# Performance work log

Measured on AMD Instinct MI355X. Metric: run time of the kernel, lower is better.

## Reference

```python
import jax, jax.numpy as jnp
import numpy as np

B, R, N = 1, 1024, 128
C_FEAT, C_MSA, C_PAIR = 22, 256, 128
NBINS = 65  # relpos bins, vbins = arange(65) - 32


def setup_inputs() -> dict:
    key = jax.random.key(0)
    ks = jax.random.split(key, 9)
    w = lambda k, shape: (jax.random.normal(k, shape, jnp.float32) * 0.05)
    return {
        "target_feat": jax.random.normal(ks[0], (B, R, C_FEAT), jnp.float32),
        "residue_index": jnp.broadcast_to(jnp.arange(R, dtype=jnp.int32), (B, R)),
        "msa_feat": jax.random.normal(ks[1], (B, N, R, C_FEAT), jnp.float32),
        "Wa": w(ks[2], (C_PAIR, C_FEAT)), "ba": jnp.zeros((C_PAIR,), jnp.float32),
        "Wb": w(ks[3], (C_PAIR, C_FEAT)), "bb": jnp.zeros((C_PAIR,), jnp.float32),
        "Wm1": w(ks[4], (C_MSA, C_FEAT)), "bm1": jnp.zeros((C_MSA,), jnp.float32),
        "Wm2": w(ks[5], (C_MSA, C_FEAT)), "bm2": jnp.zeros((C_MSA,), jnp.float32),
        "Wpos": w(ks[6], (C_PAIR, NBINS)), "bpos": jnp.zeros((C_PAIR,), jnp.float32),
    }


def reference(target_feat, residue_index, msa_feat,
              Wa, ba, Wb, bb, Wm1, bm1, Wm2, bm2, Wpos, bpos):
    # pair init: z[b,i,j] = to_a(tf)[b,j] + to_b(tf)[b,i]
    a = target_feat @ Wa.T + ba                      # (b, r, c_pair)
    bv = target_feat @ Wb.T + bb                     # (b, r, c_pair)
    z = a[:, None, :, :] + bv[:, :, None, :]         # (b, r, r, c_pair)

    # relpos: nearest-bin one-hot of d = ri[j] - ri[i] against arange(65)-32,
    # then Linear(65 -> c_pair).  One-hot @ W.T is exactly an embedding gather
    # of row clip(d+32, 0, 64) from Wpos.T, so skip materializing the one-hot.
    d = residue_index[:, None, :] - residue_index[:, :, None]  # (b, r, r)
    bins = jnp.clip(d + (NBINS // 2), 0, NBINS - 1)            # (b, r, r) int
    z = z + Wpos.T[bins] + bpos                                # gather + bias

    # MSA init: m = to_m1(msa_feat) + to_m2(target_feat) broadcast over n rows
    m = (msa_feat @ Wm1.T + bm1) + (target_feat @ Wm2.T + bm2)[:, None, :, :]
    return m, z
```

## Files before the change

kernel.cpp:

```cpp
#include <hip/hip_runtime.h>

#define RR     1024
#define NSEQ   128
#define CFEAT  22
#define CMSA   256
#define CPAIR  128
#define NBINS  65

typedef float f4 __attribute__((ext_vector_type(4)));
typedef float f2 __attribute__((ext_vector_type(2)));

__global__ __launch_bounds__(256) void k_pre(
    const float* __restrict__ tf,
    const float* __restrict__ Wa, const float* __restrict__ ba,
    const float* __restrict__ Wb, const float* __restrict__ bb,
    const float* __restrict__ Wm2, const float* __restrict__ bm2,
    const float* __restrict__ Wpos, const float* __restrict__ bpos,
    float* __restrict__ a, float* __restrict__ bvp,
    float* __restrict__ tm2, float* __restrict__ pose)
{
    __shared__ float wlds[CFEAT][512];
    __shared__ float rows[8][CFEAT];
    const int t = threadIdx.x;
    const int r0 = blockIdx.x * 8;

    for (int idx = t; idx < 128 * CFEAT; idx += 256) {
        int c = idx / CFEAT, k = idx - c * CFEAT;
        wlds[k][c] = Wa[idx];
    }
    for (int idx = t; idx < 128 * CFEAT; idx += 256) {
        int c = idx / CFEAT, k = idx - c * CFEAT;
        wlds[k][128 + c] = Wb[idx];
    }
    for (int idx = t; idx < 256 * CFEAT; idx += 256) {
        int c = idx / CFEAT, k = idx - c * CFEAT;
        wlds[k][256 + c] = Wm2[idx];
    }
    for (int idx = t; idx < 8 * CFEAT; idx += 256) {
        int rr = idx / CFEAT, k = idx - rr * CFEAT;
        rows[rr][k] = tf[(r0 + rr) * CFEAT + k];
    }
    __syncthreads();

    #pragma unroll
    for (int rr = 0; rr < 8; ++rr) {
        const int r = r0 + rr;
        float s1 = 0.f, s2 = 0.f;
        #pragma unroll
        for (int k = 0; k < CFEAT; ++k) {
            float rv = rows[rr][k];
            s1 += rv * wlds[k][t];
            s2 += rv * wlds[k][256 + t];
        }
        tm2[r * CMSA + t] = s2 + bm2[t];
        if (t < CPAIR) a[r * CPAIR + t] = s1 + ba[t];
        else           bvp[r * CPAIR + (t - CPAIR)] = s1 + bb[t - CPAIR];
    }

    if (blockIdx.x < NBINS && t < CPAIR)
        pose[blockIdx.x * CPAIR + t] = Wpos[t * NBINS + blockIdx.x] + bpos[t];
}

#define PPB 64

__global__ __launch_bounds__(256, 8) void k_fused(
    const int* __restrict__ resi,
    const float* __restrict__ a, const float* __restrict__ bvp,
    const float* __restrict__ pose, float* __restrict__ out_z,
    const float* __restrict__ msa,
    const float* __restrict__ Wm1, const float* __restrict__ bm1,
    const float* __restrict__ tm2, float* __restrict__ out_m)
{
    __shared__ union U {
        struct { float rows[PPB][24]; } m;
        struct { int rj[512]; } p;
    } sm;
    const int bx = blockIdx.x;
    const int grp = bx >> 3, sub = bx & 7;
    const int id = (grp >> 1) * 8 + sub;
    const int t = threadIdx.x;

    if ((grp & 1) == 0) {
        const int i = id >> 1;
        const int jbase = (id & 1) * 512;
        for (int idx = t; idx < 512; idx += 256)
            sm.p.rj[idx] = resi[jbase + idx];
        __syncthreads();

        const int c4 = (t & 31) * 4;
        const int jo = t >> 5;
        const int ri = resi[i];
        const f4 bvv = *(const f4*)(bvp + (long)i * CPAIR + c4);
        float* dst = out_z + ((long)i * RR + jbase) * CPAIR;

        #pragma unroll 4
        for (int jj = 0; jj < 512; jj += 8) {
            const int jl = jj + jo;
            int d = sm.p.rj[jl] - ri + (NBINS / 2);
            d = min(max(d, 0), NBINS - 1);
            const f4 av = *(const f4*)(a + (long)(jbase + jl) * CPAIR + c4);
            const f4 pv = *(const f4*)(pose + (long)d * CPAIR + c4);
            f4 o = av + bvv + pv;
            __builtin_nontemporal_store(o, (f4*)(dst + (long)jl * CPAIR + c4));
        }
    } else {
        const long pbase = (long)id * PPB;
        const float* src = msa + pbase * CFEAT;
        for (int idx = t; idx < PPB * CFEAT; idx += 256) {
            int p = idx / CFEAT, k = idx - p * CFEAT;
            sm.m.rows[p][k] = src[idx];
        }
        if (t < PPB) { sm.m.rows[t][22] = 0.f; sm.m.rows[t][23] = 0.f; }

        const int c2 = (t & 127) * 2;
        const int ps = t >> 7;
        float wA[24], wB[24];
        const float* wp = Wm1 + (long)c2 * CFEAT;
        #pragma unroll
        for (int k = 0; k < CFEAT; ++k) { wA[k] = wp[k]; wB[k] = wp[CFEAT + k]; }
        wA[22] = wA[23] = wB[22] = wB[23] = 0.f;
        const float b0 = bm1[c2], b1 = bm1[c2 + 1];
        __syncthreads();

        for (int it = 0; it < PPB / 2; ++it) {
            const int p = it * 2 + ps;
            const long pair = pbase + p;
            const int r = (int)(pair & (RR - 1));
            float a0 = 0.f, a1 = 0.f;
            #pragma unroll
            for (int k4 = 0; k4 < 6; ++k4) {
                f4 mv = *(const f4*)&sm.m.rows[p][k4 * 4];
                a0 += mv.x * wA[k4 * 4 + 0]; a1 += mv.x * wB[k4 * 4 + 0];
                a0 += mv.y * wA[k4 * 4 + 1]; a1 += mv.y * wB[k4 * 4 + 1];
                a0 += mv.z * wA[k4 * 4 + 2]; a1 += mv.z * wB[k4 * 4 + 2];
                a0 += mv.w * wA[k4 * 4 + 3]; a1 += mv.w * wB[k4 * 4 + 3];
            }
            const f2 t2 = *(const f2*)(tm2 + (long)r * CMSA + c2);
            f2 o;
            o.x = a0 + b0 + t2.x;
            o.y = a1 + b1 + t2.y;
            __builtin_nontemporal_store(o, (f2*)(out_m + pair * CMSA + c2));
        }
    }
}

extern "C" void kernel_launch(void* const* d_in, const int* in_sizes, int n_in,
                              void* d_out, int out_size, void* d_ws, size_t ws_size,
                              hipStream_t stream) {
    const float* tf   = (const float*)d_in[0];
    const int*   resi = (const int*)  d_in[1];
    const float* msa  = (const float*)d_in[2];
    const float* Wa   = (const float*)d_in[3];
    const float* ba   = (const float*)d_in[4];
    const float* Wb   = (const float*)d_in[5];
    const float* bb   = (const float*)d_in[6];
    const float* Wm1  = (const float*)d_in[7];
    const float* bm1  = (const float*)d_in[8];
    const float* Wm2  = (const float*)d_in[9];
    const float* bm2  = (const float*)d_in[10];
    const float* Wpos = (const float*)d_in[11];
    const float* bpos = (const float*)d_in[12];

    float* out_m = (float*)d_out;
    float* out_z = out_m + (long)NSEQ * RR * CMSA;

    float* a    = (float*)d_ws;
    float* bvp  = a   + (long)RR * CPAIR;
    float* tm2  = bvp + (long)RR * CPAIR;
    float* pose = tm2 + (long)RR * CMSA;

    k_pre<<<128, 256, 0, stream>>>(tf, Wa, ba, Wb, bb, Wm2, bm2, Wpos, bpos,
                                   a, bvp, tm2, pose);
    k_fused<<<4096, 256, 0, stream>>>(resi, a, bvp, pose, out_z,
                                      msa, Wm1, bm1, tm2, out_m);
}
```

Before: 148.7 us.

## Tile pair init into 16x32 blocks with a and pose staged in LDS

The z-path block now covers a 16(i) x 32(j) tile instead of one row i with 512 j. It stages the 32 rows of a and the whole 65x128 pose table in shared memory and reuses them across 16 i rows, which cuts repeated global and L2 reads of a and pose. It also swaps nontemporal stores for normal stores and drops the occupancy hint from the launch bounds. The roughly 50 KB of LDS per block lowers occupancy, and since the kernel is dominated by output writes the gain from fewer reads may be small.

```diff
diff --git a/kernel.cpp b/kernel.cpp
--- a/kernel.cpp
+++ b/kernel.cpp
@@ -63,7 +63,7 @@
 
 #define PPB 64
 
-__global__ __launch_bounds__(256, 8) void k_fused(
+__global__ __launch_bounds__(256) void k_fused(
     const int* __restrict__ resi,
     const float* __restrict__ a, const float* __restrict__ bvp,
     const float* __restrict__ pose, float* __restrict__ out_z,
@@ -72,8 +72,13 @@
     const float* __restrict__ tm2, float* __restrict__ out_m)
 {
     __shared__ union U {
+        struct {
+            float aL[32 * CPAIR];
+            float poseL[NBINS * CPAIR];
+            int   rjL[32];
+            int   riL[16];
+        } p;
         struct { float rows[PPB][24]; } m;
-        struct { int rj[512]; } p;
     } sm;
     const int bx = blockIdx.x;
     const int grp = bx >> 3, sub = bx & 7;
@@ -81,27 +86,35 @@
     const int t = threadIdx.x;
 
     if ((grp & 1) == 0) {
-        const int i = id >> 1;
-        const int jbase = (id & 1) * 512;
-        for (int idx = t; idx < 512; idx += 256)
-            sm.p.rj[idx] = resi[jbase + idx];
+        const int i0 = (id >> 5) * 16;
+        const int j0 = (id & 31) * 32;
+
+        for (int idx = t; idx < 32 * CPAIR / 4; idx += 256)
+            ((f4*)sm.p.aL)[idx] = ((const f4*)(a + (long)j0 * CPAIR))[idx];
+        for (int idx = t; idx < NBINS * CPAIR / 4; idx += 256)
+            ((f4*)sm.p.poseL)[idx] = ((const f4*)pose)[idx];
+        if (t < 32) sm.p.rjL[t] = resi[j0 + t];
+        if (t < 16) sm.p.riL[t] = resi[i0 + t];
         __syncthreads();
 
-        const int c4 = (t & 31) * 4;
+        const int cb = (t & 31) * 4;
         const int jo = t >> 5;
-        const int ri = resi[i];
-        const f4 bvv = *(const f4*)(bvp + (long)i * CPAIR + c4);
-        float* dst = out_z + ((long)i * RR + jbase) * CPAIR;
 
-        #pragma unroll 4
-        for (int jj = 0; jj < 512; jj += 8) {
-            const int jl = jj + jo;
-            int d = sm.p.rj[jl] - ri + (NBINS / 2);
-            d = min(max(d, 0), NBINS - 1);
-            const f4 av = *(const f4*)(a + (long)(jbase + jl) * CPAIR + c4);
-            const f4 pv = *(const f4*)(pose + (long)d * CPAIR + c4);
-            f4 o = av + bvv + pv;
-            __builtin_nontemporal_store(o, (f4*)(dst + (long)jl * CPAIR + c4));
+        for (int ii = 0; ii < 16; ++ii) {
+            const int i = i0 + ii;
+            const f4 bvv = *(const f4*)(bvp + (long)i * CPAIR + cb);
+            const int ri = sm.p.riL[ii];
+            float* dst = out_z + ((long)i * RR + j0) * CPAIR;
+            #pragma unroll
+            for (int q = 0; q < 4; ++q) {
+                const int jl = q * 8 + jo;
+                int d = sm.p.rjL[jl] - ri + (NBINS / 2);
+                d = min(max(d, 0), NBINS - 1);
+                const f4 av = *(const f4*)&sm.p.aL[jl * CPAIR + cb];
+                const f4 pv = *(const f4*)&sm.p.poseL[d * CPAIR + cb];
+                f4 o = av + bvv + pv;
+                *(f4*)(dst + jl * CPAIR + cb) = o;
+            }
         }
     } else {
         const long pbase = (long)id * PPB;
```

New measurement: 178.6 us. 20.1% more time.

## Merge pre and fused kernels into one persistent cooperative kernel with grid sync

Applied to the files above, without the earlier changes.

Replaces the two launches with one cooperative kernel. The first 128 blocks compute the a/b/tm2 projections, now holding weights in registers instead of LDS, and a grid-wide sync separates that phase from a persistent grid-stride loop over the 4096 work units. This removes one launch and the inter-kernel gap. In exchange it adds a grid barrier and caps the grid at the occupancy limit, so blocks loop over units instead of being scheduled by hardware.

```diff
diff --git a/kernel.cpp b/kernel.cpp
--- a/kernel.cpp
+++ b/kernel.cpp
@@ -1,4 +1,7 @@
 #include <hip/hip_runtime.h>
+#include <hip/hip_cooperative_groups.h>
+
+namespace cg = cooperative_groups;
 
 #define RR     1024
 #define NSEQ   128
@@ -6,140 +9,133 @@
 #define CMSA   256
 #define CPAIR  128
 #define NBINS  65
+#define PPB    64
+#define NUNITS 4096
 
 typedef float f4 __attribute__((ext_vector_type(4)));
 typedef float f2 __attribute__((ext_vector_type(2)));
 
-__global__ __launch_bounds__(256) void k_pre(
-    const float* __restrict__ tf,
+__global__ __launch_bounds__(256, 8) void k_all(
+    const float* __restrict__ tf, const int* __restrict__ resi,
+    const float* __restrict__ msa,
     const float* __restrict__ Wa, const float* __restrict__ ba,
     const float* __restrict__ Wb, const float* __restrict__ bb,
+    const float* __restrict__ Wm1, const float* __restrict__ bm1,
     const float* __restrict__ Wm2, const float* __restrict__ bm2,
     const float* __restrict__ Wpos, const float* __restrict__ bpos,
     float* __restrict__ a, float* __restrict__ bvp,
-    float* __restrict__ tm2, float* __restrict__ pose)
-{
-    __shared__ float wlds[CFEAT][512];
-    __shared__ float rows[8][CFEAT];
-    const int t = threadIdx.x;
-    const int r0 = blockIdx.x * 8;
-
-    for (int idx = t; idx < 128 * CFEAT; idx += 256) {
-        int c = idx / CFEAT, k = idx - c * CFEAT;
-        wlds[k][c] = Wa[idx];
-    }
-    for (int idx = t; idx < 128 * CFEAT; idx += 256) {
-        int c = idx / CFEAT, k = idx - c * CFEAT;
-        wlds[k][128 + c] = Wb[idx];
-    }
-    for (int idx = t; idx < 256 * CFEAT; idx += 256) {
-        int c = idx / CFEAT, k = idx - c * CFEAT;
-        wlds[k][256 + c] = Wm2[idx];
-    }
-    for (int idx = t; idx < 8 * CFEAT; idx += 256) {
-        int rr = idx / CFEAT, k = idx - rr * CFEAT;
-        rows[rr][k] = tf[(r0 + rr) * CFEAT + k];
-    }
-    __syncthreads();
-
-    #pragma unroll
-    for (int rr = 0; rr < 8; ++rr) {
-        const int r = r0 + rr;
-        float s1 = 0.f, s2 = 0.f;
-        #pragma unroll
-        for (int k = 0; k < CFEAT; ++k) {
-            float rv = rows[rr][k];
-            s1 += rv * wlds[k][t];
-            s2 += rv * wlds[k][256 + t];
-        }
-        tm2[r * CMSA + t] = s2 + bm2[t];
-        if (t < CPAIR) a[r * CPAIR + t] = s1 + ba[t];
-        else           bvp[r * CPAIR + (t - CPAIR)] = s1 + bb[t - CPAIR];
-    }
-
-    if (blockIdx.x < NBINS && t < CPAIR)
-        pose[blockIdx.x * CPAIR + t] = Wpos[t * NBINS + blockIdx.x] + bpos[t];
-}
-
-#define PPB 64
-
-__global__ __launch_bounds__(256, 8) void k_fused(
-    const int* __restrict__ resi,
-    const float* __restrict__ a, const float* __restrict__ bvp,
-    const float* __restrict__ pose, float* __restrict__ out_z,
-    const float* __restrict__ msa,
-    const float* __restrict__ Wm1, const float* __restrict__ bm1,
-    const float* __restrict__ tm2, float* __restrict__ out_m)
+    float* __restrict__ tm2, float* __restrict__ pose,
+    float* __restrict__ out_z, float* __restrict__ out_m)
 {
     __shared__ union U {
+        float rows8[8][CFEAT];
+        struct { int rj[512]; } p;
         struct { float rows[PPB][24]; } m;
-        struct { int rj[512]; } p;
     } sm;
-    const int bx = blockIdx.x;
-    const int grp = bx >> 3, sub = bx & 7;
-    const int id = (grp >> 1) * 8 + sub;
     const int t = threadIdx.x;
+    const int b = blockIdx.x;
 
-    if ((grp & 1) == 0) {
-        const int i = id >> 1;
-        const int jbase = (id & 1) * 512;
-        for (int idx = t; idx < 512; idx += 256)
-            sm.p.rj[idx] = resi[jbase + idx];
+    if (b < 128) {
+        const int r0 = b * 8;
+        for (int idx = t; idx < 8 * CFEAT; idx += 256)
+            sm.rows8[idx / CFEAT][idx % CFEAT] = tf[r0 * CFEAT + idx];
         __syncthreads();
 
-        const int c4 = (t & 31) * 4;
-        const int jo = t >> 5;
-        const int ri = resi[i];
-        const f4 bvv = *(const f4*)(bvp + (long)i * CPAIR + c4);
-        float* dst = out_z + ((long)i * RR + jbase) * CPAIR;
+        float w1[CFEAT], w2[CFEAT];
+        const float* wp1 = (t < CPAIR) ? (Wa + t * CFEAT)
+                                       : (Wb + (t - CPAIR) * CFEAT);
+        const float* wp2 = Wm2 + t * CFEAT;
+        #pragma unroll
+        for (int k = 0; k < CFEAT; ++k) { w1[k] = wp1[k]; w2[k] = wp2[k]; }
+        const float bias1 = (t < CPAIR) ? ba[t] : bb[t - CPAIR];
+        const float bias2 = bm2[t];
 
-        #pragma unroll 4
-        for (int jj = 0; jj < 512; jj += 8) {
-            const int jl = jj + jo;
-            int d = sm.p.rj[jl] - ri + (NBINS / 2);
-            d = min(max(d, 0), NBINS - 1);
-            const f4 av = *(const f4*)(a + (long)(jbase + jl) * CPAIR + c4);
-            const f4 pv = *(const f4*)(pose + (long)d * CPAIR + c4);
-            f4 o = av + bvv + pv;
-            __builtin_nontemporal_store(o, (f4*)(dst + (long)jl * CPAIR + c4));
+        #pragma unroll
+        for (int rr = 0; rr < 8; ++rr) {
+            float s1 = 0.f, s2 = 0.f;
+            #pragma unroll
+            for (int k = 0; k < CFEAT; ++k) {
+                const float rv = sm.rows8[rr][k];
+                s1 += rv * w1[k];
+                s2 += rv * w2[k];
+            }
+            const int r = r0 + rr;
+            tm2[r * CMSA + t] = s2 + bias2;
+            if (t < CPAIR) a[r * CPAIR + t] = s1 + bias1;
+            else           bvp[r * CPAIR + (t - CPAIR)] = s1 + bias1;
         }
-    } else {
-        const long pbase = (long)id * PPB;
-        const float* src = msa + pbase * CFEAT;
-        for (int idx = t; idx < PPB * CFEAT; idx += 256) {
-            int p = idx / CFEAT, k = idx - p * CFEAT;
-            sm.m.rows[p][k] = src[idx];
-        }
-        if (t < PPB) { sm.m.rows[t][22] = 0.f; sm.m.rows[t][23] = 0.f; }
+    }
+    if (b < NBINS && t < CPAIR)
+        pose[b * CPAIR + t] = Wpos[t * NBINS + b] + bpos[t];
 
-        const int c2 = (t & 127) * 2;
-        const int ps = t >> 7;
-        float wA[24], wB[24];
-        const float* wp = Wm1 + (long)c2 * CFEAT;
-        #pragma unroll
-        for (int k = 0; k < CFEAT; ++k) { wA[k] = wp[k]; wB[k] = wp[CFEAT + k]; }
-        wA[22] = wA[23] = wB[22] = wB[23] = 0.f;
-        const float b0 = bm1[c2], b1 = bm1[c2 + 1];
+    cg::this_grid().sync();
+
+    for (int u = b; u < NUNITS; u += gridDim.x) {
         __syncthreads();
+        const int grp = u >> 3, sub = u & 7;
+        const int id = (grp >> 1) * 8 + sub;
 
-        for (int it = 0; it < PPB / 2; ++it) {
-            const int p = it * 2 + ps;
-            const long pair = pbase + p;
-            const int r = (int)(pair & (RR - 1));
-            float a0 = 0.f, a1 = 0.f;
+        if ((grp & 1) == 0) {
+            const int i = id >> 1;
+            const int jbase = (id & 1) * 512;
+            for (int idx = t; idx < 512; idx += 256)
+                sm.p.rj[idx] = resi[jbase + idx];
+            __syncthreads();
+
+            const int c4 = (t & 31) * 4;
+            const int jo = t >> 5;
+            const int ri = resi[i];
+            const f4 bvv = *(const f4*)(bvp + (long)i * CPAIR + c4);
+            float* dst = out_z + ((long)i * RR + jbase) * CPAIR;
+
+            #pragma unroll 4
+            for (int jj = 0; jj < 512; jj += 8) {
+                const int jl = jj + jo;
+                int d = sm.p.rj[jl] - ri + (NBINS / 2);
+                d = min(max(d, 0), NBINS - 1);
+                const f4 av = *(const f4*)(a + (long)(jbase + jl) * CPAIR + c4);
+                const f4 pv = *(const f4*)(pose + (long)d * CPAIR + c4);
+                f4 o = av + bvv + pv;
+                __builtin_nontemporal_store(o, (f4*)(dst + (long)jl * CPAIR + c4));
+            }
+        } else {
+            const long pbase = (long)id * PPB;
+            const float* src = msa + pbase * CFEAT;
+            for (int idx = t; idx < PPB * CFEAT; idx += 256) {
+                int p = idx / CFEAT, k = idx - p * CFEAT;
+                sm.m.rows[p][k] = src[idx];
+            }
+            if (t < PPB) { sm.m.rows[t][22] = 0.f; sm.m.rows[t][23] = 0.f; }
+
+            const int c2 = (t & 127) * 2;
+            const int ps = t >> 7;
+            float wA[24], wB[24];
+            const float* wp = Wm1 + (long)c2 * CFEAT;
             #pragma unroll
-            for (int k4 = 0; k4 < 6; ++k4) {
-                f4 mv = *(const f4*)&sm.m.rows[p][k4 * 4];
-                a0 += mv.x * wA[k4 * 4 + 0]; a1 += mv.x * wB[k4 * 4 + 0];
-                a0 += mv.y * wA[k4 * 4 + 1]; a1 += mv.y * wB[k4 * 4 + 1];
-                a0 += mv.z * wA[k4 * 4 + 2]; a1 += mv.z * wB[k4 * 4 + 2];
-                a0 += mv.w * wA[k4 * 4 + 3]; a1 += mv.w * wB[k4 * 4 + 3];
+            for (int k = 0; k < CFEAT; ++k) { wA[k] = wp[k]; wB[k] = wp[CFEAT + k]; }
+            wA[22] = wA[23] = wB[22] = wB[23] = 0.f;
+            const float b0 = bm1[c2], b1 = bm1[c2 + 1];
+            __syncthreads();
+
+            for (int it = 0; it < PPB / 2; ++it) {
+                const int p = it * 2 + ps;
+                const long pair = pbase + p;
+                const int r = (int)(pair & (RR - 1));
+                float a0 = 0.f, a1 = 0.f;
+                #pragma unroll
+                for (int k4 = 0; k4 < 6; ++k4) {
+                    f4 mv = *(const f4*)&sm.m.rows[p][k4 * 4];
+                    a0 += mv.x * wA[k4 * 4 + 0]; a1 += mv.x * wB[k4 * 4 + 0];
+                    a0 += mv.y * wA[k4 * 4 + 1]; a1 += mv.y * wB[k4 * 4 + 1];
+                    a0 += mv.z * wA[k4 * 4 + 2]; a1 += mv.z * wB[k4 * 4 + 2];
+                    a0 += mv.w * wA[k4 * 4 + 3]; a1 += mv.w * wB[k4 * 4 + 3];
+                }
+                const f2 t2 = *(const f2*)(tm2 + (long)r * CMSA + c2);
+                f2 o;
+                o.x = a0 + b0 + t2.x;
+                o.y = a1 + b1 + t2.y;
+                __builtin_nontemporal_store(o, (f2*)(out_m + pair * CMSA + c2));
             }
-            const f2 t2 = *(const f2*)(tm2 + (long)r * CMSA + c2);
-            f2 o;
-            o.x = a0 + b0 + t2.x;
-            o.y = a1 + b1 + t2.y;
-            __builtin_nontemporal_store(o, (f2*)(out_m + pair * CMSA + c2));
         }
     }
 }
@@ -169,8 +165,21 @@
     float* tm2  = bvp + (long)RR * CPAIR;
     float* pose = tm2 + (long)RR * CMSA;
 
-    k_pre<<<128, 256, 0, stream>>>(tf, Wa, ba, Wb, bb, Wm2, bm2, Wpos, bpos,
-                                   a, bvp, tm2, pose);
-    k_fused<<<4096, 256, 0, stream>>>(resi, a, bvp, pose, out_z,
-                                      msa, Wm1, bm1, tm2, out_m);
+    int occ = 8;
+    (void)hipOccupancyMaxActiveBlocksPerMultiprocessor(&occ, (const void*)k_all,
+                                                       256, 0);
+    int grid = occ * 256;
+    if (grid > 2048) grid = 2048;
+    if (grid > NUNITS) grid = NUNITS;
+
+    void* args[] = {
+        (void*)&tf, (void*)&resi, (void*)&msa,
+        (void*)&Wa, (void*)&ba, (void*)&Wb, (void*)&bb,
+        (void*)&Wm1, (void*)&bm1, (void*)&Wm2, (void*)&bm2,
+        (void*)&Wpos, (void*)&bpos,
+        (void*)&a, (void*)&bvp, (void*)&tm2, (void*)&pose,
+        (void*)&out_z, (void*)&out_m,
+    };
+    (void)hipLaunchCooperativeKernel((const void*)k_all, dim3(grid), dim3(256),
+                                     args, 0, stream);
 }
```

New measurement: 272.9 us. 83.5% more time.

## Switch fused kernel to persistent blocks with interleaved pair/MSA work split

Applied to the files above, without the earlier changes.

Cuts the grid from 4096 to 1280 blocks that loop over more work each. 1024 blocks handle pair output in 512-float chunks strided across the whole z tensor, and 256 blocks each process 512 MSA rows in eight 64-row LDS segments, reusing Wm1 registers across segments. The aim is to amortise per-block setup (weight loads, LDS staging) and shift the pair/MSA mix from 1:1 to 4:1. In exchange, pair blocks now read resi and bvp from global memory on every iteration, and the occupancy hint is removed from launch bounds.

```diff
diff --git a/kernel.cpp b/kernel.cpp
--- a/kernel.cpp
+++ b/kernel.cpp
@@ -61,9 +61,7 @@
         pose[blockIdx.x * CPAIR + t] = Wpos[t * NBINS + blockIdx.x] + bpos[t];
 }
 
-#define PPB 64
-
-__global__ __launch_bounds__(256, 8) void k_fused(
+__global__ __launch_bounds__(256) void k_fused(
     const int* __restrict__ resi,
     const float* __restrict__ a, const float* __restrict__ bvp,
     const float* __restrict__ pose, float* __restrict__ out_z,
@@ -71,47 +69,33 @@
     const float* __restrict__ Wm1, const float* __restrict__ bm1,
     const float* __restrict__ tm2, float* __restrict__ out_m)
 {
-    __shared__ union U {
-        struct { float rows[PPB][24]; } m;
-        struct { int rj[512]; } p;
-    } sm;
-    const int bx = blockIdx.x;
-    const int grp = bx >> 3, sub = bx & 7;
-    const int id = (grp >> 1) * 8 + sub;
+    __shared__ float rows[64][24];
+    const int b = blockIdx.x;
     const int t = threadIdx.x;
+    const int q = b >> 3, s = b & 7;
+    const int q5 = q / 5, qm = q - q5 * 5;
 
-    if ((grp & 1) == 0) {
-        const int i = id >> 1;
-        const int jbase = (id & 1) * 512;
-        for (int idx = t; idx < 512; idx += 256)
-            sm.p.rj[idx] = resi[jbase + idx];
-        __syncthreads();
-
+    if (qm < 4) {
+        const int pid = (q5 * 4 + qm) * 8 + s;
         const int c4 = (t & 31) * 4;
         const int jo = t >> 5;
-        const int ri = resi[i];
-        const f4 bvv = *(const f4*)(bvp + (long)i * CPAIR + c4);
-        float* dst = out_z + ((long)i * RR + jbase) * CPAIR;
 
-        #pragma unroll 4
-        for (int jj = 0; jj < 512; jj += 8) {
-            const int jl = jj + jo;
-            int d = sm.p.rj[jl] - ri + (NBINS / 2);
+        #pragma unroll 2
+        for (int n = 0; n < 128; ++n) {
+            const int chunk = n * 1024 + pid;
+            const int i = chunk >> 7;
+            const int j = ((chunk & 127) << 3) + jo;
+            int d = resi[j] - resi[i] + (NBINS / 2);
             d = min(max(d, 0), NBINS - 1);
-            const f4 av = *(const f4*)(a + (long)(jbase + jl) * CPAIR + c4);
-            const f4 pv = *(const f4*)(pose + (long)d * CPAIR + c4);
+            const f4 bvv = *(const f4*)(bvp + (long)i * CPAIR + c4);
+            const f4 av  = *(const f4*)(a + (long)j * CPAIR + c4);
+            const f4 pv  = *(const f4*)(pose + (long)d * CPAIR + c4);
             f4 o = av + bvv + pv;
-            __builtin_nontemporal_store(o, (f4*)(dst + (long)jl * CPAIR + c4));
+            __builtin_nontemporal_store(
+                o, (f4*)(out_z + ((long)i * RR + j) * CPAIR + c4));
         }
     } else {
-        const long pbase = (long)id * PPB;
-        const float* src = msa + pbase * CFEAT;
-        for (int idx = t; idx < PPB * CFEAT; idx += 256) {
-            int p = idx / CFEAT, k = idx - p * CFEAT;
-            sm.m.rows[p][k] = src[idx];
-        }
-        if (t < PPB) { sm.m.rows[t][22] = 0.f; sm.m.rows[t][23] = 0.f; }
-
+        const int mid = q5 * 8 + s;
         const int c2 = (t & 127) * 2;
         const int ps = t >> 7;
         float wA[24], wB[24];
@@ -120,26 +104,37 @@
         for (int k = 0; k < CFEAT; ++k) { wA[k] = wp[k]; wB[k] = wp[CFEAT + k]; }
         wA[22] = wA[23] = wB[22] = wB[23] = 0.f;
         const float b0 = bm1[c2], b1 = bm1[c2 + 1];
-        __syncthreads();
 
-        for (int it = 0; it < PPB / 2; ++it) {
-            const int p = it * 2 + ps;
-            const long pair = pbase + p;
-            const int r = (int)(pair & (RR - 1));
-            float a0 = 0.f, a1 = 0.f;
-            #pragma unroll
-            for (int k4 = 0; k4 < 6; ++k4) {
-                f4 mv = *(const f4*)&sm.m.rows[p][k4 * 4];
-                a0 += mv.x * wA[k4 * 4 + 0]; a1 += mv.x * wB[k4 * 4 + 0];
-                a0 += mv.y * wA[k4 * 4 + 1]; a1 += mv.y * wB[k4 * 4 + 1];
-                a0 += mv.z * wA[k4 * 4 + 2]; a1 += mv.z * wB[k4 * 4 + 2];
-                a0 += mv.w * wA[k4 * 4 + 3]; a1 += mv.w * wB[k4 * 4 + 3];
+        for (int seg = 0; seg < 8; ++seg) {
+            const long pbase = (long)mid * 512 + seg * 64;
+            __syncthreads();
+            const float* src = msa + pbase * CFEAT;
+            for (int idx = t; idx < 64 * CFEAT; idx += 256) {
+                int p = idx / CFEAT, k = idx - p * CFEAT;
+                rows[p][k] = src[idx];
             }
-            const f2 t2 = *(const f2*)(tm2 + (long)r * CMSA + c2);
-            f2 o;
-            o.x = a0 + b0 + t2.x;
-            o.y = a1 + b1 + t2.y;
-            __builtin_nontemporal_store(o, (f2*)(out_m + pair * CMSA + c2));
+            if (t < 64) { rows[t][22] = 0.f; rows[t][23] = 0.f; }
+            __syncthreads();
+
+            for (int it = 0; it < 32; ++it) {
+                const int p = it * 2 + ps;
+                const long pair = pbase + p;
+                const int r = (int)(pair & (RR - 1));
+                float a0 = 0.f, a1 = 0.f;
+                #pragma unroll
+                for (int k4 = 0; k4 < 6; ++k4) {
+                    f4 mv = *(const f4*)&rows[p][k4 * 4];
+                    a0 += mv.x * wA[k4 * 4 + 0]; a1 += mv.x * wB[k4 * 4 + 0];
+                    a0 += mv.y * wA[k4 * 4 + 1]; a1 += mv.y * wB[k4 * 4 + 1];
+                    a0 += mv.z * wA[k4 * 4 + 2]; a1 += mv.z * wB[k4 * 4 + 2];
+                    a0 += mv.w * wA[k4 * 4 + 3]; a1 += mv.w * wB[k4 * 4 + 3];
+                }
+                const f2 t2 = *(const f2*)(tm2 + (long)r * CMSA + c2);
+                f2 o;
+                o.x = a0 + b0 + t2.x;
+                o.y = a1 + b1 + t2.y;
+                __builtin_nontemporal_store(o, (f2*)(out_m + pair * CMSA + c2));
+            }
         }
     }
 }
@@ -171,6 +166,6 @@
 
     k_pre<<<128, 256, 0, stream>>>(tf, Wa, ba, Wb, bb, Wm2, bm2, Wpos, bpos,
                                    a, bvp, tm2, pose);
-    k_fused<<<4096, 256, 0, stream>>>(resi, a, bvp, pose, out_z,
+    k_fused<<<1280, 256, 0, stream>>>(resi, a, bvp, pose, out_z,
                                       msa, Wm1, bm1, tm2, out_m);
 }
```

Result: slower. 168.7 us (+13.4%).
